# Optimization experiments

Measured on AMD Instinct MI355X. Metric: run time of the kernel, lower is better.

## Reference

```python
import jax, jax.numpy as jnp
import numpy as np

N_NODES = 100000
N_EDGES = 600000
D_IN = 128
D_OUT = 128
N_REL = 16
N_BASES = 8


def setup_inputs() -> dict:
    key = jax.random.key(0)
    ks = jax.random.split(key, 6)
    x = jax.random.normal(ks[0], (N_NODES, D_IN), dtype=jnp.float32)
    edge_index = jax.random.randint(ks[1], (2, N_EDGES), 0, N_NODES, dtype=jnp.int64)
    edge_type = jax.random.randint(ks[2], (N_EDGES,), 0, N_REL, dtype=jnp.int64)
    # xavier-uniform-ish init scales
    b_lim = float(np.sqrt(6.0 / (D_IN + D_OUT)))
    c_lim = float(np.sqrt(6.0 / (N_REL + N_BASES)))
    w_lim = float(np.sqrt(6.0 / (D_IN + D_OUT)))
    bases = jax.random.uniform(ks[3], (N_BASES, D_IN, D_OUT), jnp.float32, -b_lim, b_lim)
    coefficients = jax.random.uniform(ks[4], (N_REL, N_BASES), jnp.float32, -c_lim, c_lim)
    w_self = jax.random.uniform(ks[5], (D_OUT, D_IN), jnp.float32, -w_lim, w_lim)
    return {"x": x, "edge_index": edge_index, "edge_type": edge_type,
            "bases": bases, "coefficients": coefficients, "w_self": w_self}


def reference(x, edge_index, edge_type, bases, coefficients, w_self):
    # self loop: Linear(in, out, bias=False) -> x @ W^T
    out = x @ w_self.T  # [N, D_OUT]
    # relation weights from basis decomposition
    weights = jnp.einsum('rb,bio->rio', coefficients, bases)  # [R, D_IN, D_OUT]
    row, col = edge_index[0], edge_index[1]
    xc = x[col]  # [E, D_IN] gather of source features
    n_rel = weights.shape[0]
    msg = jnp.zeros((xc.shape[0], w_self.shape[0]), dtype=x.dtype)
    # fixed small loop over relations; masked accumulate matches per-relation grouped GEMM
    for r in range(n_rel):
        sel = (edge_type == r)[:, None]
        msg = msg + jnp.where(sel, xc @ weights[r], jnp.zeros((), x.dtype))
    # scatter-add messages to destination rows
    out = out.at[row].add(msg)
    return out
```

## Files before the change

kernel.cpp:

```cpp
#include <hip/hip_runtime.h>

#define NN 100000
#define NE 600000
#define ET (NE + NN)
#define D 128
#define NREL 16
#define SCANB 391
#define MAXTILES 10954
#define GEMMG MAXTILES
#define WGRID 1088

typedef short short8 __attribute__((ext_vector_type(8)));
typedef float f32x4 __attribute__((ext_vector_type(4)));
typedef unsigned int u32x4 __attribute__((ext_vector_type(4)));

#define C0 0
#define O0 20
#define CU0 40
#define T0 60

#define WT_OFF   0
#define META_OFF 557056
#define DH_OFF   557568
#define DO_OFF   957568
#define DC_OFF   1357576
#define BS_OFF   1757576
#define SCP_OFF  1759576
#define SR_OFF   7360088
#define XB_OFF   10160096
#define MSGB_OFF 35760096
#define MSGA_OFF 10160096
#define NEED_B   (MSGB_OFF + (size_t)ET * 128 * 2)
#define NEED_A   (MSGA_OFF + (size_t)ET * 128 * 2)

__device__ __forceinline__ unsigned short f2bf(float f) {
  unsigned u = __builtin_bit_cast(unsigned, f);
  u += 0x7fffu + ((u >> 16) & 1u);
  return (unsigned short)(u >> 16);
}

__device__ __forceinline__ void lds_barrier() {
  asm volatile("s_waitcnt lgkmcnt(0)" ::: "memory");
  __builtin_amdgcn_s_barrier();
}

__global__ __launch_bounds__(256) void k_prep(const float* __restrict__ bases,
    const float* __restrict__ coef, const float* __restrict__ w_self,
    unsigned short* __restrict__ wT, const float* __restrict__ x,
    unsigned short* __restrict__ xb)
{
  if (blockIdx.x < WGRID) {
    int idx = blockIdx.x * 256 + threadIdx.x;
    int r = idx >> 14;
    int t = idx & 16383;
    float v;
    if (r < 16) {
      int o = t >> 7, i = t & 127;
      float acc = 0.f;
      #pragma unroll
      for (int b = 0; b < 8; ++b)
        acc += coef[r * 8 + b] * bases[b * 16384 + i * 128 + o];
      v = acc;
    } else {
      v = w_self[t];
    }
    wT[idx] = f2bf(v);
  } else {
    int i = (blockIdx.x - WGRID) * 256 + threadIdx.x;
    if (i >= NN * D / 4) return;
    f32x4 f = __builtin_nontemporal_load((const f32x4*)(x + (size_t)i * 4));
    unsigned short s0 = f2bf(f[0]), s1 = f2bf(f[1]), s2 = f2bf(f[2]), s3 = f2bf(f[3]);
    unsigned long long pk = (unsigned long long)s0 | ((unsigned long long)s1 << 16)
                          | ((unsigned long long)s2 << 32) | ((unsigned long long)s3 << 48);
    *(unsigned long long*)(xb + (size_t)i * 4) = pk;
  }
}

__global__ __launch_bounds__(256) void k_hist(const int* __restrict__ ei,
    const int* __restrict__ et, int* __restrict__ meta, int* __restrict__ dstHist)
{
  __shared__ int h[16];
  int tid = threadIdx.x;
  if (tid < 16) h[tid] = 0;
  __syncthreads();
  for (int e = blockIdx.x * 256 + tid; e < NE; e += gridDim.x * 256) {
    atomicAdd(&h[et[e]], 1);
    atomicAdd(&dstHist[ei[e]], 1);
  }
  __syncthreads();
  if (tid < 16) atomicAdd(&meta[C0 + tid], h[tid]);
}

__global__ __launch_bounds__(256) void k_scan1(const int* __restrict__ dstHist,
    int* __restrict__ dstOff, int* __restrict__ blockSums)
{
  __shared__ int sh[256];
  int tid = threadIdx.x;
  int d = blockIdx.x * 256 + tid;
  int v = (d < NN) ? (dstHist[d] + 1) : 0;
  sh[tid] = v;
  __syncthreads();
  #pragma unroll
  for (int ofs = 1; ofs < 256; ofs <<= 1) {
    int t = (tid >= ofs) ? sh[tid - ofs] : 0;
    __syncthreads();
    sh[tid] += t;
    __syncthreads();
  }
  if (d < NN) dstOff[d] = sh[tid] - v;
  if (tid == 255) blockSums[blockIdx.x] = sh[tid];
}

__global__ __launch_bounds__(512) void k_scan2(int* __restrict__ blockSums, int* __restrict__ meta)
{
  __shared__ int sh[512];
  int tid = threadIdx.x;
  int v = (tid < SCANB) ? blockSums[tid] : 0;
  sh[tid] = v;
  __syncthreads();
  #pragma unroll
  for (int ofs = 1; ofs < 512; ofs <<= 1) {
    int t = (tid >= ofs) ? sh[tid - ofs] : 0;
    __syncthreads();
    sh[tid] += t;
    __syncthreads();
  }
  if (tid == 0) {
    meta[C0 + 16] = NN;
    int off = 0, toff = 0;
    for (int r = 0; r <= 16; ++r) {
      meta[O0 + r] = off;
      meta[CU0 + r] = off;
      meta[T0 + r] = toff;
      int c = meta[C0 + r];
      off += c;
      toff += (c + 63) >> 6;
    }
    meta[O0 + 17] = off;
    meta[T0 + 17] = toff;
  }
  if (tid < SCANB) blockSums[tid] = sh[tid] - v;
}

__global__ __launch_bounds__(256) void k_scan3(int* __restrict__ dstOff,
    const int* __restrict__ blockSums, int* __restrict__ dstCursor,
    int2* __restrict__ sCP)
{
  int tid = threadIdx.x;
  int d = blockIdx.x * 256 + tid;
  int base = blockSums[blockIdx.x];
  if (d < NN) {
    int o = dstOff[d] + base;
    dstOff[d] = o;
    dstCursor[d] = o + 1;
    sCP[NE + d] = make_int2(d, o);
  }
  if (d == NN) dstOff[NN] = ET;
}

__global__ __launch_bounds__(256) void k_self0(int2* __restrict__ sCP, int* __restrict__ sRow)
{
  int n = blockIdx.x * 256 + threadIdx.x;
  if (n < NN) { sCP[NE + n] = make_int2(n, 0); sRow[NE + n] = n; }
}

__global__ __launch_bounds__(256) void k_scatter(const int* __restrict__ ei, const int* __restrict__ et,
    int* __restrict__ meta, int2* __restrict__ sCP, int* __restrict__ sRow,
    int* __restrict__ dstCursor, int doMsg)
{
  __shared__ int h[16], base[16], lh[16];
  int tid = threadIdx.x;
  int start = blockIdx.x * 4096;
  int end = min(NE, start + 4096);
  if (tid < 16) { h[tid] = 0; lh[tid] = 0; }
  __syncthreads();
  for (int e = start + tid; e < end; e += 256)
    atomicAdd(&h[et[e]], 1);
  __syncthreads();
  if (tid < 16) base[tid] = atomicAdd(&meta[CU0 + tid], h[tid]);
  __syncthreads();
  for (int e = start + tid; e < end; e += 256) {
    int r = et[e];
    int row = ei[e];
    int pos = base[r] + atomicAdd(&lh[r], 1);
    int slot = doMsg ? atomicAdd(&dstCursor[row], 1) : 0;
    sCP[pos] = make_int2(ei[NE + e], slot);
    if (!doMsg) sRow[pos] = row;
  }
}

__global__ __launch_bounds__(256) void k_gemm(const float* __restrict__ xf,
    const unsigned short* __restrict__ xb,
    const unsigned short* __restrict__ wT, const int* __restrict__ meta,
    const int2* __restrict__ sCP, const int* __restrict__ sRow,
    unsigned short* __restrict__ msg, float* __restrict__ out,
    int xbf, int msgmode)
{
  __shared__ short As[64 * 17 * 8];
  __shared__ int Pos[64];
  __shared__ int Rows[64];
  __shared__ int Ms[80];

  int tid = threadIdx.x;
  if (tid < 80) Ms[tid] = meta[tid];
  __syncthreads();
  int ntiles = Ms[T0 + 17];
  int b = blockIdx.x;
  if (b >= ntiles) return;

  int lane = tid & 63, wave = tid >> 6;
  int q = lane >> 4, l15 = lane & 15;
  int m = tid >> 2, ug = tid & 3;

  int r = 0;
  while (r < 16 && Ms[T0 + r + 1] <= b) ++r;
  int boff = Ms[O0 + r];
  int e0 = boff + (b - Ms[T0 + r]) * 64;
  int nr = min(64, boff + Ms[C0 + r] - e0);

  bool valid = m < nr;
  int e = valid ? (e0 + m) : e0;
  int2 cp = sCP[e];
  if (ug == 0) {
    Pos[m] = valid ? cp.y : 0;
    if (!msgmode) Rows[m] = valid ? sRow[e] : 0;
  }

  if (xbf) {
    const unsigned short* xr = xb + (size_t)cp.x * 128;
    #pragma unroll
    for (int s = 0; s < 4; ++s) {
      int u = ug * 4 + s;
      short8 pk = (short8)(short)0;
      if (valid) pk = *(const short8*)(xr + u * 8);
      *(short8*)&As[(m * 17 + u) * 8] = pk;
    }
  } else {
    const float* xr = xf + (size_t)cp.x * 128;
    #pragma unroll
    for (int s = 0; s < 4; ++s) {
      int u = ug * 4 + s;
      float4 f0 = make_float4(0.f, 0.f, 0.f, 0.f), f1 = f0;
      if (valid) {
        f0 = *(const float4*)(xr + u * 8);
        f1 = *(const float4*)(xr + u * 8 + 4);
      }
      short8 pk;
      pk[0] = (short)f2bf(f0.x); pk[1] = (short)f2bf(f0.y);
      pk[2] = (short)f2bf(f0.z); pk[3] = (short)f2bf(f0.w);
      pk[4] = (short)f2bf(f1.x); pk[5] = (short)f2bf(f1.y);
      pk[6] = (short)f2bf(f1.z); pk[7] = (short)f2bf(f1.w);
      *(short8*)&As[(m * 17 + u) * 8] = pk;
    }
  }

  short8 bfr[2][4];
  {
    const unsigned short* wr = wT + r * 16384;
    #pragma unroll
    for (int ns = 0; ns < 2; ++ns)
      #pragma unroll
      for (int kk = 0; kk < 4; ++kk)
        bfr[ns][kk] = *(const short8*)(wr + (wave * 32 + ns * 16 + l15) * 128 + kk * 32 + q * 8);
  }

  lds_barrier();

  f32x4 acc[4][2];
  #pragma unroll
  for (int ms = 0; ms < 4; ++ms)
    #pragma unroll
    for (int ns = 0; ns < 2; ++ns)
      acc[ms][ns] = (f32x4){0.f, 0.f, 0.f, 0.f};
  #pragma unroll
  for (int kk = 0; kk < 4; ++kk) {
    short8 af[4];
    #pragma unroll
    for (int ms = 0; ms < 4; ++ms)
      af[ms] = *(const short8*)&As[((ms * 16 + l15) * 17 + kk * 4 + q) * 8];
    #pragma unroll
    for (int ms = 0; ms < 4; ++ms)
      #pragma unroll
      for (int ns = 0; ns < 2; ++ns)
        acc[ms][ns] = __builtin_amdgcn_mfma_f32_16x16x32_bf16(af[ms], bfr[ns][kk], acc[ms][ns], 0, 0, 0);
  }

  if (msgmode) {
    #pragma unroll
    for (int ms = 0; ms < 4; ++ms)
      #pragma unroll
      for (int reg = 0; reg < 4; ++reg) {
        int erow = ms * 16 + q * 4 + reg;
        if (erow < nr) {
          unsigned short* mp = msg + (size_t)Pos[erow] * 128 + wave * 32 + l15;
          mp[0]  = f2bf(acc[ms][0][reg]);
          mp[16] = f2bf(acc[ms][1][reg]);
        }
      }
  } else {
    #pragma unroll
    for (int ms = 0; ms < 4; ++ms)
      #pragma unroll
      for (int reg = 0; reg < 4; ++reg) {
        int erow = ms * 16 + q * 4 + reg;
        if (erow < nr) {
          float* op = out + (size_t)Rows[erow] * 128 + wave * 32 + l15;
          unsafeAtomicAdd(op, acc[ms][0][reg]);
          unsafeAtomicAdd(op + 16, acc[ms][1][reg]);
        }
      }
  }
}

__global__ __launch_bounds__(256) void k_reduce(const unsigned short* __restrict__ msg,
    const int* __restrict__ dstOff, float* __restrict__ out)
{
  int d = blockIdx.x * 16 + (threadIdx.x >> 4);
  if (d >= NN) return;
  int sl = threadIdx.x & 15;
  int s = dstOff[d], e = dstOff[d + 1];
  const unsigned short* base = msg + (size_t)sl * 8;
  float a[8], bacc[8];
  #pragma unroll
  for (int i = 0; i < 8; ++i) { a[i] = 0.f; bacc[i] = 0.f; }
  int j = s;
  for (; j + 1 < e; j += 2) {
    u32x4 v0 = __builtin_nontemporal_load((const u32x4*)(base + (size_t)j * 128));
    u32x4 v1 = __builtin_nontemporal_load((const u32x4*)(base + (size_t)(j + 1) * 128));
    #pragma unroll
    for (int c = 0; c < 4; ++c) {
      a[2 * c]     += __builtin_bit_cast(float, v0[c] << 16);
      a[2 * c + 1] += __builtin_bit_cast(float, v0[c] & 0xffff0000u);
      bacc[2 * c]     += __builtin_bit_cast(float, v1[c] << 16);
      bacc[2 * c + 1] += __builtin_bit_cast(float, v1[c] & 0xffff0000u);
    }
  }
  if (j < e) {
    u32x4 v0 = __builtin_nontemporal_load((const u32x4*)(base + (size_t)j * 128));
    #pragma unroll
    for (int c = 0; c < 4; ++c) {
      a[2 * c]     += __builtin_bit_cast(float, v0[c] << 16);
      a[2 * c + 1] += __builtin_bit_cast(float, v0[c] & 0xffff0000u);
    }
  }
  f32x4 w0, w1;
  w0[0] = a[0] + bacc[0]; w0[1] = a[1] + bacc[1]; w0[2] = a[2] + bacc[2]; w0[3] = a[3] + bacc[3];
  w1[0] = a[4] + bacc[4]; w1[1] = a[5] + bacc[5]; w1[2] = a[6] + bacc[6]; w1[3] = a[7] + bacc[7];
  float* op = out + (size_t)d * 128 + sl * 8;
  __builtin_nontemporal_store(w0, (f32x4*)op);
  __builtin_nontemporal_store(w1, (f32x4*)(op + 4));
}

extern "C" void kernel_launch(void* const* d_in, const int* in_sizes, int n_in,
                              void* d_out, int out_size, void* d_ws, size_t ws_size,
                              hipStream_t stream)
{
  const float* x      = (const float*)d_in[0];
  const int*   ei     = (const int*)d_in[1];
  const int*   et     = (const int*)d_in[2];
  const float* bases  = (const float*)d_in[3];
  const float* coef   = (const float*)d_in[4];
  const float* w_self = (const float*)d_in[5];
  float* out = (float*)d_out;
  char* ws = (char*)d_ws;
  unsigned short* wT = (unsigned short*)(ws + WT_OFF);
  int* meta      = (int*)(ws + META_OFF);
  int* dstHist   = (int*)(ws + DH_OFF);
  int* dstOff    = (int*)(ws + DO_OFF);
  int* dstCursor = (int*)(ws + DC_OFF);
  int* blockSums = (int*)(ws + BS_OFF);
  int2* sCP      = (int2*)(ws + SCP_OFF);
  int* sRow      = (int*)(ws + SR_OFF);
  unsigned short* xb = (unsigned short*)(ws + XB_OFF);

  const int modeB = (ws_size >= NEED_B) ? 1 : 0;
  const int modeA = (modeB || ws_size >= NEED_A) ? 1 : 0;
  unsigned short* msg = (unsigned short*)(ws + (modeB ? MSGB_OFF : MSGA_OFF));

  hipMemsetAsync(ws + META_OFF, 0, 512 + 400000, stream);
  k_prep<<<modeB ? (WGRID + 12500) : WGRID, 256, 0, stream>>>(bases, coef, w_self, wT, x, xb);
  k_hist<<<256, 256, 0, stream>>>(ei, et, meta, dstHist);
  if (modeA) {
    k_scan1<<<SCANB, 256, 0, stream>>>(dstHist, dstOff, blockSums);
    k_scan2<<<1, 512, 0, stream>>>(blockSums, meta);
    k_scan3<<<SCANB, 256, 0, stream>>>(dstOff, blockSums, dstCursor, sCP);
  } else {
    k_scan2<<<1, 512, 0, stream>>>(blockSums, meta);
    k_self0<<<SCANB, 256, 0, stream>>>(sCP, sRow);
    hipMemsetAsync(d_out, 0, (size_t)NN * D * 4, stream);
  }
  k_scatter<<<(NE + 4095) / 4096, 256, 0, stream>>>(ei, et, meta, sCP, sRow, dstCursor, modeA);
  k_gemm<<<GEMMG, 256, 0, stream>>>(x, xb, wT, meta, sCP, sRow, msg, out, modeB, modeA);
  if (modeA)
    k_reduce<<<(NN + 15) / 16, 256, 0, stream>>>(msg, dstOff, out);
}
```

Measured before the change: 328.8 us.

## Replace bf16 message buffer and segmented reduce with direct fp32 atomic scatter

Removes the destination histogram, three-pass scan, per-destination slot assignment, bf16 message staging buffer and k_reduce kernel. The GEMM epilogue now atomically adds fp32 results straight into a zeroed output, with the destination row packed into sCP. This drops a large write and read of messages and several launches. In exchange it relies on heavy global float atomics with contention on popular rows, adds a full memset of the output, and makes summation order nondeterministic.

```diff
diff --git a/kernel.cpp b/kernel.cpp
--- a/kernel.cpp
+++ b/kernel.cpp
@@ -7,12 +7,10 @@
 #define NREL 16
 #define SCANB 391
 #define MAXTILES 10954
-#define GEMMG MAXTILES
 #define WGRID 1088
 
 typedef short short8 __attribute__((ext_vector_type(8)));
 typedef float f32x4 __attribute__((ext_vector_type(4)));
-typedef unsigned int u32x4 __attribute__((ext_vector_type(4)));
 
 #define C0 0
 #define O0 20
@@ -21,17 +19,9 @@
 
 #define WT_OFF   0
 #define META_OFF 557056
-#define DH_OFF   557568
-#define DO_OFF   957568
-#define DC_OFF   1357576
-#define BS_OFF   1757576
-#define SCP_OFF  1759576
-#define SR_OFF   7360088
-#define XB_OFF   10160096
-#define MSGB_OFF 35760096
-#define MSGA_OFF 10160096
-#define NEED_B   (MSGB_OFF + (size_t)ET * 128 * 2)
-#define NEED_A   (MSGA_OFF + (size_t)ET * 128 * 2)
+#define SCP_OFF  557568
+#define XB_OFF   6158080
+#define NEED_XB  (XB_OFF + (size_t)NN * D * 2)
 
 __device__ __forceinline__ unsigned short f2bf(float f) {
   unsigned u = __builtin_bit_cast(unsigned, f);
@@ -76,56 +66,22 @@
   }
 }
 
-__global__ __launch_bounds__(256) void k_hist(const int* __restrict__ ei,
-    const int* __restrict__ et, int* __restrict__ meta, int* __restrict__ dstHist)
+__global__ __launch_bounds__(256) void k_hist(const int* __restrict__ et,
+    int* __restrict__ meta)
 {
   __shared__ int h[16];
   int tid = threadIdx.x;
   if (tid < 16) h[tid] = 0;
   __syncthreads();
-  for (int e = blockIdx.x * 256 + tid; e < NE; e += gridDim.x * 256) {
+  for (int e = blockIdx.x * 256 + tid; e < NE; e += gridDim.x * 256)
     atomicAdd(&h[et[e]], 1);
-    atomicAdd(&dstHist[ei[e]], 1);
-  }
   __syncthreads();
   if (tid < 16) atomicAdd(&meta[C0 + tid], h[tid]);
 }
 
-__global__ __launch_bounds__(256) void k_scan1(const int* __restrict__ dstHist,
-    int* __restrict__ dstOff, int* __restrict__ blockSums)
-{
-  __shared__ int sh[256];
-  int tid = threadIdx.x;
-  int d = blockIdx.x * 256 + tid;
-  int v = (d < NN) ? (dstHist[d] + 1) : 0;
-  sh[tid] = v;
-  __syncthreads();
-  #pragma unroll
-  for (int ofs = 1; ofs < 256; ofs <<= 1) {
-    int t = (tid >= ofs) ? sh[tid - ofs] : 0;
-    __syncthreads();
-    sh[tid] += t;
-    __syncthreads();
-  }
-  if (d < NN) dstOff[d] = sh[tid] - v;
-  if (tid == 255) blockSums[blockIdx.x] = sh[tid];
-}
-
-__global__ __launch_bounds__(512) void k_scan2(int* __restrict__ blockSums, int* __restrict__ meta)
-{
-  __shared__ int sh[512];
-  int tid = threadIdx.x;
-  int v = (tid < SCANB) ? blockSums[tid] : 0;
-  sh[tid] = v;
-  __syncthreads();
-  #pragma unroll
-  for (int ofs = 1; ofs < 512; ofs <<= 1) {
-    int t = (tid >= ofs) ? sh[tid - ofs] : 0;
-    __syncthreads();
-    sh[tid] += t;
-    __syncthreads();
-  }
-  if (tid == 0) {
+__global__ __launch_bounds__(64) void k_meta(int* __restrict__ meta)
+{
+  if (threadIdx.x == 0) {
     meta[C0 + 16] = NN;
     int off = 0, toff = 0;
     for (int r = 0; r <= 16; ++r) {
@@ -139,34 +95,16 @@
     meta[O0 + 17] = off;
     meta[T0 + 17] = toff;
   }
-  if (tid < SCANB) blockSums[tid] = sh[tid] - v;
-}
-
-__global__ __launch_bounds__(256) void k_scan3(int* __restrict__ dstOff,
-    const int* __restrict__ blockSums, int* __restrict__ dstCursor,
-    int2* __restrict__ sCP)
-{
-  int tid = threadIdx.x;
-  int d = blockIdx.x * 256 + tid;
-  int base = blockSums[blockIdx.x];
-  if (d < NN) {
-    int o = dstOff[d] + base;
-    dstOff[d] = o;
-    dstCursor[d] = o + 1;
-    sCP[NE + d] = make_int2(d, o);
-  }
-  if (d == NN) dstOff[NN] = ET;
-}
-
-__global__ __launch_bounds__(256) void k_self0(int2* __restrict__ sCP, int* __restrict__ sRow)
+}
+
+__global__ __launch_bounds__(256) void k_self0(int2* __restrict__ sCP)
 {
   int n = blockIdx.x * 256 + threadIdx.x;
-  if (n < NN) { sCP[NE + n] = make_int2(n, 0); sRow[NE + n] = n; }
+  if (n < NN) sCP[NE + n] = make_int2(n, n);
 }
 
 __global__ __launch_bounds__(256) void k_scatter(const int* __restrict__ ei, const int* __restrict__ et,
-    int* __restrict__ meta, int2* __restrict__ sCP, int* __restrict__ sRow,
-    int* __restrict__ dstCursor, int doMsg)
+    int* __restrict__ meta, int2* __restrict__ sCP)
 {
   __shared__ int h[16], base[16], lh[16];
   int tid = threadIdx.x;
@@ -181,23 +119,17 @@
   __syncthreads();
   for (int e = start + tid; e < end; e += 256) {
     int r = et[e];
-    int row = ei[e];
     int pos = base[r] + atomicAdd(&lh[r], 1);
-    int slot = doMsg ? atomicAdd(&dstCursor[row], 1) : 0;
-    sCP[pos] = make_int2(ei[NE + e], slot);
-    if (!doMsg) sRow[pos] = row;
+    sCP[pos] = make_int2(ei[NE + e], ei[e]);
   }
 }
 
 __global__ __launch_bounds__(256) void k_gemm(const float* __restrict__ xf,
     const unsigned short* __restrict__ xb,
     const unsigned short* __restrict__ wT, const int* __restrict__ meta,
-    const int2* __restrict__ sCP, const int* __restrict__ sRow,
-    unsigned short* __restrict__ msg, float* __restrict__ out,
-    int xbf, int msgmode)
+    const int2* __restrict__ sCP, float* __restrict__ out, int xbf)
 {
   __shared__ short As[64 * 17 * 8];
-  __shared__ int Pos[64];
   __shared__ int Rows[64];
   __shared__ int Ms[80];
 
@@ -221,10 +153,7 @@
   bool valid = m < nr;
   int e = valid ? (e0 + m) : e0;
   int2 cp = sCP[e];
-  if (ug == 0) {
-    Pos[m] = valid ? cp.y : 0;
-    if (!msgmode) Rows[m] = valid ? sRow[e] : 0;
-  }
+  if (ug == 0) Rows[m] = valid ? cp.y : 0;
 
   if (xbf) {
     const unsigned short* xr = xb + (size_t)cp.x * 128;
@@ -285,70 +214,17 @@
         acc[ms][ns] = __builtin_amdgcn_mfma_f32_16x16x32_bf16(af[ms], bfr[ns][kk], acc[ms][ns], 0, 0, 0);
   }
 
-  if (msgmode) {
-    #pragma unroll
-    for (int ms = 0; ms < 4; ++ms)
-      #pragma unroll
-      for (int reg = 0; reg < 4; ++reg) {
-        int erow = ms * 16 + q * 4 + reg;
-        if (erow < nr) {
-          unsigned short* mp = msg + (size_t)Pos[erow] * 128 + wave * 32 + l15;
-          mp[0]  = f2bf(acc[ms][0][reg]);
-          mp[16] = f2bf(acc[ms][1][reg]);
-        }
+  #pragma unroll
+  for (int ms = 0; ms < 4; ++ms)
+    #pragma unroll
+    for (int reg = 0; reg < 4; ++reg) {
+      int erow = ms * 16 + q * 4 + reg;
+      if (erow < nr) {
+        float* op = out + (size_t)Rows[erow] * 128 + wave * 32 + l15;
+        unsafeAtomicAdd(op, acc[ms][0][reg]);
+        unsafeAtomicAdd(op + 16, acc[ms][1][reg]);
       }
-  } else {
-    #pragma unroll
-    for (int ms = 0; ms < 4; ++ms)
-      #pragma unroll
-      for (int reg = 0; reg < 4; ++reg) {
-        int erow = ms * 16 + q * 4 + reg;
-        if (erow < nr) {
-          float* op = out + (size_t)Rows[erow] * 128 + wave * 32 + l15;
-          unsafeAtomicAdd(op, acc[ms][0][reg]);
-          unsafeAtomicAdd(op + 16, acc[ms][1][reg]);
-        }
-      }
-  }
-}
-
-__global__ __launch_bounds__(256) void k_reduce(const unsigned short* __restrict__ msg,
-    const int* __restrict__ dstOff, float* __restrict__ out)
-{
-  int d = blockIdx.x * 16 + (threadIdx.x >> 4);
-  if (d >= NN) return;
-  int sl = threadIdx.x & 15;
-  int s = dstOff[d], e = dstOff[d + 1];
-  const unsigned short* base = msg + (size_t)sl * 8;
-  float a[8], bacc[8];
-  #pragma unroll
-  for (int i = 0; i < 8; ++i) { a[i] = 0.f; bacc[i] = 0.f; }
-  int j = s;
-  for (; j + 1 < e; j += 2) {
-    u32x4 v0 = __builtin_nontemporal_load((const u32x4*)(base + (size_t)j * 128));
-    u32x4 v1 = __builtin_nontemporal_load((const u32x4*)(base + (size_t)(j + 1) * 128));
-    #pragma unroll
-    for (int c = 0; c < 4; ++c) {
-      a[2 * c]     += __builtin_bit_cast(float, v0[c] << 16);
-      a[2 * c + 1] += __builtin_bit_cast(float, v0[c] & 0xffff0000u);
-      bacc[2 * c]     += __builtin_bit_cast(float, v1[c] << 16);
-      bacc[2 * c + 1] += __builtin_bit_cast(float, v1[c] & 0xffff0000u);
-    }
-  }
-  if (j < e) {
-    u32x4 v0 = __builtin_nontemporal_load((const u32x4*)(base + (size_t)j * 128));
-    #pragma unroll
-    for (int c = 0; c < 4; ++c) {
-      a[2 * c]     += __builtin_bit_cast(float, v0[c] << 16);
-      a[2 * c + 1] += __builtin_bit_cast(float, v0[c] & 0xffff0000u);
-    }
-  }
-  f32x4 w0, w1;
-  w0[0] = a[0] + bacc[0]; w0[1] = a[1] + bacc[1]; w0[2] = a[2] + bacc[2]; w0[3] = a[3] + bacc[3];
-  w1[0] = a[4] + bacc[4]; w1[1] = a[5] + bacc[5]; w1[2] = a[6] + bacc[6]; w1[3] = a[7] + bacc[7];
-  float* op = out + (size_t)d * 128 + sl * 8;
-  __builtin_nontemporal_store(w0, (f32x4*)op);
-  __builtin_nontemporal_store(w1, (f32x4*)(op + 4));
+    }
 }
 
 extern "C" void kernel_launch(void* const* d_in, const int* in_sizes, int n_in,
@@ -365,32 +241,17 @@
   char* ws = (char*)d_ws;
   unsigned short* wT = (unsigned short*)(ws + WT_OFF);
   int* meta      = (int*)(ws + META_OFF);
-  int* dstHist   = (int*)(ws + DH_OFF);
-  int* dstOff    = (int*)(ws + DO_OFF);
-  int* dstCursor = (int*)(ws + DC_OFF);
-  int* blockSums = (int*)(ws + BS_OFF);
   int2* sCP      = (int2*)(ws + SCP_OFF);
-  int* sRow      = (int*)(ws + SR_OFF);
   unsigned short* xb = (unsigned short*)(ws + XB_OFF);
 
-  const int modeB = (ws_size >= NEED_B) ? 1 : 0;
-  const int modeA = (modeB || ws_size >= NEED_A) ? 1 : 0;
-  unsigned short* msg = (unsigned short*)(ws + (modeB ? MSGB_OFF : MSGA_OFF));
-
-  hipMemsetAsync(ws + META_OFF, 0, 512 + 400000, stream);
-  k_prep<<<modeB ? (WGRID + 12500) : WGRID, 256, 0, stream>>>(bases, coef, w_self, wT, x, xb);
-  k_hist<<<256, 256, 0, stream>>>(ei, et, meta, dstHist);
-  if (modeA) {
-    k_scan1<<<SCANB, 256, 0, stream>>>(dstHist, dstOff, blockSums);
-    k_scan2<<<1, 512, 0, stream>>>(blockSums, meta);
-    k_scan3<<<SCANB, 256, 0, stream>>>(dstOff, blockSums, dstCursor, sCP);
-  } else {
-    k_scan2<<<1, 512, 0, stream>>>(blockSums, meta);
-    k_self0<<<SCANB, 256, 0, stream>>>(sCP, sRow);
-    hipMemsetAsync(d_out, 0, (size_t)NN * D * 4, stream);
-  }
-  k_scatter<<<(NE + 4095) / 4096, 256, 0, stream>>>(ei, et, meta, sCP, sRow, dstCursor, modeA);
-  k_gemm<<<GEMMG, 256, 0, stream>>>(x, xb, wT, meta, sCP, sRow, msg, out, modeB, modeA);
-  if (modeA)
-    k_reduce<<<(NN + 15) / 16, 256, 0, stream>>>(msg, dstOff, out);
-}
+  const int xbf = (ws_size >= NEED_XB) ? 1 : 0;
+
+  hipMemsetAsync(ws + META_OFF, 0, 512, stream);
+  hipMemsetAsync(d_out, 0, (size_t)NN * D * 4, stream);
+  k_prep<<<xbf ? (WGRID + 12500) : WGRID, 256, 0, stream>>>(bases, coef, w_self, wT, x, xb);
+  k_hist<<<256, 256, 0, stream>>>(et, meta);
+  k_meta<<<1, 64, 0, stream>>>(meta);
+  k_self0<<<SCANB, 256, 0, stream>>>(sCP);
+  k_scatter<<<(NE + 4095) / 4096, 256, 0, stream>>>(ei, et, meta, sCP);
+  k_gemm<<<MAXTILES, 256, 0, stream>>>(x, xb, wT, meta, sCP, out, xbf);
+}
```

After: 438.0 us. 1.33x slower.
